# Kernel tuning notes

Measured on AMD Instinct MI355X. Metric: run time of the kernel, lower is better.

## Reference

```python
import jax, jax.numpy as jnp
import numpy as np
from jax import lax

STATE_LEN = 5
N_BASE = 4
N_STATES = N_BASE ** STATE_LEN      # 1024
ALPHA_LEN = N_BASE + 1              # 5 (blank + 4 bases)
BLANK_SCORE = 2.0
SCALE = 5.0
NEG = -1e30                         # log-zero surrogate (avoids -inf NaNs)

def _make_idx():
    s = np.arange(N_STATES)
    stay = s[:, None]
    # torch: arange(1024).repeat_interleave(4).reshape(4,-1).T -> idx[j,1+b] = b*256 + j//4
    move = np.repeat(s, N_BASE).reshape(N_BASE, -1).T
    return jnp.asarray(np.concatenate([stay, move], axis=1), dtype=jnp.int32)  # (1024,5)

IDX = _make_idx()

def _logZ_full(scores):
    # full-lattice logZ; scores (T,N,5120)
    T, N, C = scores.shape
    Ms = scores.reshape(T, N, N_STATES, ALPHA_LEN)
    def step(alpha, Mt):
        a = alpha[:, IDX]                          # (N,1024,5) gather of predecessors
        return jax.nn.logsumexp(a + Mt, axis=-1), None
    alpha0 = jnp.zeros((N, N_STATES), scores.dtype)
    alphaT, _ = lax.scan(step, alpha0, Ms)
    return jax.nn.logsumexp(alphaT, axis=-1)       # (N,)

def _prepare_ctc_scores(scores, targets):
    # scores (T,N,C), targets (N,Lmax) base ids in 1..4
    t = jnp.clip(targets - 1, 0)
    T, N, C = scores.shape
    Lmax = t.shape[1]
    n = Lmax - (STATE_LEN - 1)
    stay_idx = sum(t[:, i:n + i] * (N_BASE ** (STATE_LEN - i - 1)) for i in range(STATE_LEN)) * ALPHA_LEN
    move_idx = stay_idx[:, 1:] + t[:, :n - 1] + 1
    stay = jnp.take_along_axis(scores, jnp.broadcast_to(stay_idx[None], (T, N, n)), axis=2)
    move = jnp.take_along_axis(scores, jnp.broadcast_to(move_idx[None], (T, N, n - 1)), axis=2)
    return stay, move

def _ctc_logZ(stay, move, lens):
    # stay (T,N,L), move (T,N,L-1), lens (N,) effective kmer-path lengths
    T, N, L = stay.shape
    alpha0 = jnp.full((N, L), NEG, stay.dtype).at[:, 0].set(0.0)
    def step(alpha, sm):
        s, m = sm
        moved = jnp.pad(alpha[:, :-1] + m, ((0, 0), (1, 0)), constant_values=NEG)
        return jnp.logaddexp(alpha + s, moved), None
    alphaT, _ = lax.scan(step, alpha0, (stay, move))
    return alphaT[jnp.arange(N), lens - 1]

def setup_inputs() -> dict:
    key = jax.random.key(0)
    k1, k2, k3, k4, k5, k6 = jax.random.split(key, 6)
    B, T, D, Lmax = 16, 512, 512, 256
    hs_pad = jax.random.normal(k1, (B, T, D), dtype=jnp.float32)
    hlens = jnp.full((B,), T, dtype=jnp.int32)
    ys_pad = jax.random.randint(k2, (B, Lmax), 1, 5, dtype=jnp.int32)
    ys_lens = jax.random.randint(k3, (B,), 64, Lmax + 1, dtype=jnp.int32)
    W = jax.random.normal(k4, (4096, D), dtype=jnp.float32) * 0.02
    b = jax.random.normal(k5, (4096,), dtype=jnp.float32) * 0.01
    return {"hs_pad": hs_pad, "hlens": hlens, "ys_pad": ys_pad, "ys_lens": ys_lens, "W": W, "b": b}

def reference(hs_pad, hlens, ys_pad, ys_lens, W, b):
    x = jnp.transpose(hs_pad, (1, 0, 2))                 # (T,B,D)
    scores = jnp.tanh(x @ W.T + b) * SCALE               # (T,N,4096)
    T, N, C = scores.shape
    scores = jnp.pad(scores.reshape(T, N, C // N_BASE, N_BASE),
                     ((0, 0), (0, 0), (0, 0), (1, 0)), constant_values=BLANK_SCORE)
    scores = scores.reshape(T, N, -1).astype(jnp.float32)  # (T,N,5120)
    # normalise: subtract full-lattice logZ / T
    logZ = _logZ_full(scores)
    norm = scores - logZ[:, None] / T                    # (N,1) broadcasts over (T,N,C)
    stay, move = _prepare_ctc_scores(norm, ys_pad)
    logz = _ctc_logZ(stay, move, ys_lens + 1 - STATE_LEN)
    loss = -(logz / ys_lens.astype(scores.dtype))        # (N,) (reduction=None in forward)
    scores_bt = jnp.transpose(scores, (1, 0, 2))
    return loss, scores_bt, scores_bt
```

## Files before the change

kernel.cpp:

```cpp
#include <hip/hip_runtime.h>
#include <hip/hip_bf16.h>
#include <hip/hip_fp16.h>
#include <math.h>

#define T_STEPS 512
#define NB      16
#define D_IN    512
#define CG      4096
#define CO      5120
#define LMAX    252
#define NEGF    (-1e30f)
#define SCORES_SZ 41943040LL
#define L2E 1.4426950408889634f
#define LN2 0.6931471805599453f
#define STAYT 0.36787944117144233f

typedef __attribute__((ext_vector_type(8))) short bf16x8;
typedef __attribute__((ext_vector_type(4))) float f32x4;

__device__ __forceinline__ float tanh5(float x) {
    x = fminf(fmaxf(x, -15.f), 15.f);
    float e = __expf(2.f * x);
    return 5.f * (e - 1.f) / (e + 1.f);
}
__device__ __forceinline__ unsigned short f2bf(float v) {
    __hip_bfloat16 h = __float2bfloat16(v);
    return *reinterpret_cast<unsigned short*>(&h);
}
__device__ __forceinline__ float h2f(unsigned short s) {
    union { unsigned short u; _Float16 h; } c; c.u = s;
    return (float)c.h;
}
__device__ __forceinline__ unsigned short f2h(float v) {
    union { unsigned short u; _Float16 h; } c; c.h = (_Float16)v;
    return c.u;
}
__device__ __forceinline__ void cvt8(uint4 u, float* g) {
    g[0] = h2f((unsigned short)(u.x & 0xffff)); g[1] = h2f((unsigned short)(u.x >> 16));
    g[2] = h2f((unsigned short)(u.y & 0xffff)); g[3] = h2f((unsigned short)(u.y >> 16));
    g[4] = h2f((unsigned short)(u.z & 0xffff)); g[5] = h2f((unsigned short)(u.z >> 16));
    g[6] = h2f((unsigned short)(u.w & 0xffff)); g[7] = h2f((unsigned short)(u.w >> 16));
}
__device__ __forceinline__ void xbar() {
    __builtin_amdgcn_sched_barrier(0);
    asm volatile("s_waitcnt lgkmcnt(0)");
    __builtin_amdgcn_s_barrier();
    __builtin_amdgcn_sched_barrier(0);
}
__device__ __forceinline__ void gll16(const unsigned short* g, unsigned short* l) {
    __builtin_amdgcn_global_load_lds((const __attribute__((address_space(1))) void*)g,
                                     (__attribute__((address_space(3))) void*)l, 16, 0, 0);
}

__global__ __launch_bounds__(256) void cvt_bf16_kernel(const float* __restrict__ src,
                                                       unsigned short* __restrict__ dst,
                                                       int n4) {
    int i = blockIdx.x * 256 + threadIdx.x;
    if (i < n4) {
        float4 v = *(reinterpret_cast<const float4*>(src) + i);
        ushort4 o;
        o.x = f2bf(v.x); o.y = f2bf(v.y); o.z = f2bf(v.z); o.w = f2bf(v.w);
        *(reinterpret_cast<ushort4*>(dst) + i) = o;
    }
}

template <bool WSE>
__global__ __launch_bounds__(256) void crf_gemm_bf16(
    const unsigned short* __restrict__ A16,
    const unsigned short* __restrict__ W16,
    const float* __restrict__ bias,
    float* __restrict__ out,
    unsigned short* __restrict__ e16)
{
    __shared__ unsigned short As[128 * 64];
    __shared__ unsigned short Bs[128 * 64];
    const int tid  = threadIdx.x;
    const int lane = tid & 63;
    const int wv   = __builtin_amdgcn_readfirstlane(tid >> 6);
    const int wr   = wv >> 1, wc = wv & 1;
    const int m0   = blockIdx.y * 128;
    const int n0   = blockIdx.x * 128;
    const int wbase = tid & 192;

    f32x4 acc[4][4];
    #pragma unroll
    for (int i = 0; i < 4; ++i)
        #pragma unroll
        for (int j = 0; j < 4; ++j) acc[i][j] = (f32x4){0.f, 0.f, 0.f, 0.f};

    const int l15 = lane & 15, lj = lane >> 4, l7 = lane & 7;

    for (int k0 = 0; k0 < D_IN; k0 += 64) {
        __syncthreads();
        #pragma unroll
        for (int i = 0; i < 4; ++i) {
            const int c   = i * 256 + tid;
            const int row = c >> 3;
            const int jg  = (c & 7) ^ (row & 7);
            const unsigned short* ga = A16 + (size_t)(m0 + row) * D_IN + k0 + jg * 8;
            const unsigned short* gb = W16 + (size_t)(n0 + row) * D_IN + k0 + jg * 8;
            gll16(ga, As + (size_t)(i * 256 + wbase) * 8);
            gll16(gb, Bs + (size_t)(i * 256 + wbase) * 8);
        }
        __syncthreads();
        #pragma unroll
        for (int ks = 0; ks < 2; ++ks) {
            bf16x8 af[4], bb[4];
            #pragma unroll
            for (int mi = 0; mi < 4; ++mi) {
                const int row = wr * 64 + mi * 16 + l15;
                const int jsw = (ks * 4 + lj) ^ l7;
                af[mi] = *reinterpret_cast<const bf16x8*>(&As[row * 64 + jsw * 8]);
            }
            #pragma unroll
            for (int ni = 0; ni < 4; ++ni) {
                const int row = wc * 64 + ni * 16 + l15;
                const int jsw = (ks * 4 + lj) ^ l7;
                bb[ni] = *reinterpret_cast<const bf16x8*>(&Bs[row * 64 + jsw * 8]);
            }
            #pragma unroll
            for (int mi = 0; mi < 4; ++mi)
                #pragma unroll
                for (int ni = 0; ni < 4; ++ni)
                    acc[mi][ni] = __builtin_amdgcn_mfma_f32_16x16x32_bf16(
                        af[mi], bb[ni], acc[mi][ni], 0, 0, 0);
        }
    }

    float bv[4];
    #pragma unroll
    for (int ni = 0; ni < 4; ++ni) bv[ni] = bias[n0 + wc * 64 + ni * 16 + l15];

    #pragma unroll
    for (int mi = 0; mi < 4; ++mi) {
        #pragma unroll
        for (int r = 0; r < 4; ++r) {
            const int m = m0 + wr * 64 + mi * 16 + lj * 4 + r;
            float* r1 = out + 16 + (size_t)m * CO;
            #pragma unroll
            for (int ni = 0; ni < 4; ++ni) {
                const int n = n0 + wc * 64 + ni * 16 + l15;
                const float v = tanh5(acc[mi][ni][r] + bv[ni]);
                const int ch = (n >> 2) * 5 + (n & 3) + 1;
                r1[ch] = v;
                r1[ch + SCORES_SZ] = v;
                if ((l15 & 3) == 0) {
                    r1[ch - 1] = 2.0f;
                    r1[ch - 1 + SCORES_SZ] = 2.0f;
                }
                if (WSE) e16[(size_t)m * CG + n] = f2h(__expf(v - 3.0f));
            }
        }
    }
}

__global__ __launch_bounds__(256) void fb2_kernel(
    const unsigned short* __restrict__ e16,
    const int* __restrict__ ys_pad,
    const int* __restrict__ ys_lens,
    float* __restrict__ FA, float* __restrict__ FAe,
    float* __restrict__ FB, float* __restrict__ FBe,
    float* __restrict__ CAL, float* __restrict__ CBE)
{
    __shared__ float buf[2][1024];
    __shared__ float wmax4[4];
    __shared__ int tcl[256];
    const int role = blockIdx.x >> 4;
    const int n = blockIdx.x & 15;
    const int q = threadIdx.x;
    const int w = q >> 6, lane = q & 63;
    if (role < 2) {
        const bool FWD = (role == 0);
        const unsigned short* eb = e16 + (size_t)(n * T_STEPS) * CG + 16 * q;
        float P0 = 1.f, P1 = 1.f, P2 = 1.f, P3 = 1.f, acc = 0.f;
        *(float4*)&buf[0][4 * q] = make_float4(1.f, 1.f, 1.f, 1.f);
        uint4 pf[8][2];
        #pragma unroll
        for (int u = 0; u < 8; ++u) {
            const int row = FWD ? u : (511 - u);
            pf[u][0] = *(const uint4*)(eb + (size_t)row * CG);
            pf[u][1] = *(const uint4*)(eb + (size_t)row * CG + 8);
        }
        xbar();
        int cur = 0;
        for (int t = 0; t < 256; t += 8) {
            #pragma unroll
            for (int u = 0; u < 8; ++u) {
                float g[16];
                cvt8(pf[u][0], g);
                cvt8(pf[u][1], g + 8);
                int tn = t + u + 8; if (tn > 255) tn = 255;
                const int row = FWD ? tn : (511 - tn);
                pf[u][0] = *(const uint4*)(eb + (size_t)row * CG);
                pf[u][1] = *(const uint4*)(eb + (size_t)row * CG + 8);
                float n0, n1, n2, n3;
                if (FWD) {
                    const float b0 = buf[cur][q];
                    const float b1 = buf[cur][q + 256];
                    const float b2 = buf[cur][q + 512];
                    const float b3 = buf[cur][q + 768];
                    n0 = fmaf(STAYT, P0, fmaf(g[0],  b0, g[1]  * b1) + fmaf(g[2],  b2, g[3]  * b3));
                    n1 = fmaf(STAYT, P1, fmaf(g[4],  b0, g[5]  * b1) + fmaf(g[6],  b2, g[7]  * b3));
                    n2 = fmaf(STAYT, P2, fmaf(g[8],  b0, g[9]  * b1) + fmaf(g[10], b2, g[11] * b3));
                    n3 = fmaf(STAYT, P3, fmaf(g[12], b0, g[13] * b1) + fmaf(g[14], b2, g[15] * b3));
                } else {
                    const float4 b4 = *(const float4*)&buf[cur][4 * q];
                    n0 = fmaf(STAYT, P0, fmaf(g[0], b4.x, g[4] * b4.y) + fmaf(g[8],  b4.z, g[12] * b4.w));
                    n1 = fmaf(STAYT, P1, fmaf(g[1], b4.x, g[5] * b4.y) + fmaf(g[9],  b4.z, g[13] * b4.w));
                    n2 = fmaf(STAYT, P2, fmaf(g[2], b4.x, g[6] * b4.y) + fmaf(g[10], b4.z, g[14] * b4.w));
                    n3 = fmaf(STAYT, P3, fmaf(g[3], b4.x, g[7] * b4.y) + fmaf(g[11], b4.z, g[15] * b4.w));
                }
                if (((t + u) & 7) == 1) {
                    const float wm = fmaxf(fmaxf(wmax4[0], wmax4[1]), fmaxf(wmax4[2], wmax4[3]));
                    const int e = (int)((__float_as_uint(wm) >> 23) & 0xff) - 127;
                    const float c = __uint_as_float((unsigned)(127 - e) << 23);
                    n0 *= c; n1 *= c; n2 *= c; n3 *= c;
                    acc += (float)e;
                }
                P0 = n0; P1 = n1; P2 = n2; P3 = n3;
                if (FWD) {
                    *(float4*)&buf[cur ^ 1][4 * q] = make_float4(P0, P1, P2, P3);
                } else {
                    buf[cur ^ 1][q]       = P0;
                    buf[cur ^ 1][q + 256] = P1;
                    buf[cur ^ 1][q + 512] = P2;
                    buf[cur ^ 1][q + 768] = P3;
                }
                if (((t + u) & 7) == 0) {
                    float m = fmaxf(fmaxf(P0, P1), fmaxf(P2, P3));
                    #pragma unroll
                    for (int msk = 1; msk < 64; msk <<= 1)
                        m = fmaxf(m, __shfl_xor(m, msk, 64));
                    if (lane == 0) wmax4[w] = m;
                }
                xbar();
                cur ^= 1;
            }
        }
        if (FWD) {
            *(float4*)&FA[n * 1024 + 4 * q] = make_float4(P0, P1, P2, P3);
            if (q == 0) FAe[n] = acc;
        } else {
            FB[n * 1024 + q]       = P0;
            FB[n * 1024 + q + 256] = P1;
            FB[n * 1024 + q + 512] = P2;
            FB[n * 1024 + q + 768] = P3;
            if (q == 0) FBe[n] = acc;
        }
    } else {
        float* abuf = &buf[0][0];
        const bool FWD = (role == 2);
        tcl[q] = max(ys_pad[n * 256 + q] - 1, 0);
        xbar();
        int mch = 0; bool val;
        if (FWD) {
            val = (q >= 1 && q < LMAX);
            if (val) {
                const int code = tcl[q] * 256 + tcl[q + 1] * 64 + tcl[q + 2] * 16
                               + tcl[q + 3] * 4 + tcl[q + 4];
                mch = code * 4 + tcl[q - 1];
            }
        } else {
            val = (q < LMAX - 1);
            if (val) {
                const int code = tcl[q + 1] * 256 + tcl[q + 2] * 64 + tcl[q + 3] * 16
                               + tcl[q + 4] * 4 + tcl[q + 5];
                mch = code * 4 + tcl[q];
            }
        }
        const int li = ys_lens[n] - 5;
        float a = FWD ? ((q == 0) ? 0.f : NEGF)
                      : ((q == li) ? 0.f : NEGF);
        abuf[q] = a;
        const unsigned short* eb = e16 + (size_t)(n * T_STEPS) * CG + mch;
        unsigned short pv[16];
        #pragma unroll
        for (int s = 0; s < 16; ++s) {
            const int row = FWD ? s : (511 - s);
            pv[s] = eb[(size_t)row * CG];
        }
        xbar();
        const float STAY2 = (2.0f - 3.0f) * L2E;
        int cur = 0;
        for (int t = 0; t < 256; t += 16) {
            #pragma unroll
            for (int u = 0; u < 16; ++u) {
                const float g2 = val ? __builtin_amdgcn_logf(h2f(pv[u])) : NEGF;
                int tn = t + u + 16; if (tn > 255) tn = 255;
                const int row = FWD ? tn : (511 - tn);
                pv[u] = eb[(size_t)row * CG];
                float nb;
                if (FWD) nb = (q > 0)   ? abuf[cur * 256 + q - 1] : NEGF;
                else     nb = (q < 255) ? abuf[cur * 256 + q + 1] : NEGF;
                const float st = a + STAY2;
                const float mv = nb + g2;
                const float mx = fmaxf(st, mv);
                const float mn = fminf(st, mv);
                a = mx + __builtin_amdgcn_logf(1.f + __builtin_amdgcn_exp2f(mn - mx));
                abuf[(cur ^ 1) * 256 + q] = a;
                xbar();
                cur ^= 1;
            }
        }
        if (FWD) CAL[n * 256 + q] = a;
        else     CBE[n * 256 + q] = a;
    }
}

__global__ __launch_bounds__(256) void combine2_kernel(
    const float* __restrict__ FA, const float* __restrict__ FAe,
    const float* __restrict__ FB, const float* __restrict__ FBe,
    const float* __restrict__ CAL, const float* __restrict__ CBE,
    const int* __restrict__ ys_lens,
    float* __restrict__ out)
{
    __shared__ float red[256];
    __shared__ float lz;
    const int n = blockIdx.x;
    const int q = threadIdx.x;
    float s = 0.f;
    #pragma unroll
    for (int k = 0; k < 4; ++k)
        s += FA[n * 1024 + 4 * q + k] * FB[n * 1024 + 4 * q + k];
    red[q] = s; __syncthreads();
    for (int off = 128; off > 0; off >>= 1) {
        if (q < off) red[q] += red[q + off];
        __syncthreads();
    }
    if (q == 0) lz = FAe[n] + FBe[n] + __builtin_amdgcn_logf(red[0]);
    __syncthreads();
    const float x = CAL[n * 256 + q] + CBE[n * 256 + q];
    red[q] = x; __syncthreads();
    for (int off = 128; off > 0; off >>= 1) {
        if (q < off) red[q] = fmaxf(red[q], red[q + off]);
        __syncthreads();
    }
    const float m = red[0]; __syncthreads();
    red[q] = __builtin_amdgcn_exp2f(x - m); __syncthreads();
    for (int off = 128; off > 0; off >>= 1) {
        if (q < off) red[q] += red[q + off];
        __syncthreads();
    }
    if (q == 0) {
        const float un = m + __builtin_amdgcn_logf(red[0]);
        out[n] = -(LN2 * (un - lz) / (float)ys_lens[n]);
    }
}

__global__ __launch_bounds__(1024) void crf_fwd_kernel(
    const float* __restrict__ scores,
    const int* __restrict__ ys_pad,
    const int* __restrict__ ys_lens,
    float* __restrict__ ws)
{
    const int blk = blockIdx.x;
    const float STAY = 2.0f * L2E;
    if (blk < NB) {
        const int n = blk;
        const int s = threadIdx.x;
        __shared__ float buf[2][1024];
        __shared__ float red[1024];
        float alpha = 0.f;
        buf[0][s] = 0.f;
        const int j0 = s >> 2;
        const float* rowp = scores + (size_t)(n * T_STEPS) * CO + 5 * s + 1;
        float pm[4][4];
        #pragma unroll
        for (int u = 0; u < 4; ++u) {
            const float* r = rowp + (size_t)u * CO;
            pm[u][0] = r[0]; pm[u][1] = r[1]; pm[u][2] = r[2]; pm[u][3] = r[3];
        }
        __syncthreads();
        int cur = 0;
        for (int t = 0; t < T_STEPS; t += 4) {
            #pragma unroll
            for (int u = 0; u < 4; ++u) {
                const float m1 = pm[u][0], m2 = pm[u][1], m3 = pm[u][2], m4 = pm[u][3];
                int tp = t + u + 4; if (tp > T_STEPS - 1) tp = T_STEPS - 1;
                const float* r = rowp + (size_t)tp * CO;
                pm[u][0] = r[0]; pm[u][1] = r[1]; pm[u][2] = r[2]; pm[u][3] = r[3];
                const float b1 = buf[cur][j0];
                const float b2 = buf[cur][j0 + 256];
                const float b3 = buf[cur][j0 + 512];
                const float b4 = buf[cur][j0 + 768];
                const float a0 = alpha + STAY;
                const float a1 = fmaf(m1, L2E, b1);
                const float a2 = fmaf(m2, L2E, b2);
                const float a3 = fmaf(m3, L2E, b3);
                const float a4 = fmaf(m4, L2E, b4);
                const float mx = fmaxf(fmaxf(fmaxf(a0, a1), fmaxf(a2, a3)), a4);
                const float sum = __builtin_amdgcn_exp2f(a0 - mx) + __builtin_amdgcn_exp2f(a1 - mx)
                                + __builtin_amdgcn_exp2f(a2 - mx) + __builtin_amdgcn_exp2f(a3 - mx)
                                + __builtin_amdgcn_exp2f(a4 - mx);
                alpha = mx + __builtin_amdgcn_logf(sum);
                buf[cur ^ 1][s] = alpha;
                __syncthreads();
                cur ^= 1;
            }
        }
        red[s] = alpha;
        __syncthreads();
        for (int off = 512; off > 0; off >>= 1) {
            if (s < off) red[s] = fmaxf(red[s], red[s + off]);
            __syncthreads();
        }
        const float gmax = red[0];
        __syncthreads();
        red[s] = __builtin_amdgcn_exp2f(alpha - gmax);
        __syncthreads();
        for (int off = 512; off > 0; off >>= 1) {
            if (s < off) red[s] += red[s + off];
            __syncthreads();
        }
        if (s == 0) ws[n] = LN2 * (gmax + __builtin_amdgcn_logf(red[0]));
    } else {
        const int n = blk - NB;
        const int i = threadIdx.x;
        __shared__ float abuf[2][LMAX];
        __shared__ int tcl[256];
        if (i < 256) tcl[i] = max(ys_pad[n * 256 + i] - 1, 0);
        __syncthreads();
        int mch = -1;
        if (i >= 1 && i < LMAX) {
            const int code = tcl[i] * 256 + tcl[i + 1] * 64 + tcl[i + 2] * 16
                           + tcl[i + 3] * 4 + tcl[i + 4];
            mch = code * 5 + tcl[i - 1] + 1;
        }
        float alpha = (i == 0) ? 0.f : NEGF;
        if (i < LMAX) abuf[0][i] = alpha;
        const float* base = scores + (size_t)(n * T_STEPS) * CO;
        const size_t moff = (mch >= 0) ? (size_t)mch : 0;
        float pg[4];
        #pragma unroll
        for (int u = 0; u < 4; ++u) pg[u] = base[(size_t)u * CO + moff];
        __syncthreads();
        int cur = 0;
        for (int t = 0; t < T_STEPS; t += 4) {
            #pragma unroll
            for (int u = 0; u < 4; ++u) {
                const float g = pg[u];
                int tp = t + u + 4; if (tp > T_STEPS - 1) tp = T_STEPS - 1;
                pg[u] = base[(size_t)tp * CO + moff];
                if (i < LMAX) {
                    const float a_stay = alpha + STAY;
                    const float prev = (i > 0) ? abuf[cur][i - 1] : NEGF;
                    const float a_mv = (i > 0) ? fmaf(g, L2E, prev) : NEGF;
                    const float mx = fmaxf(a_stay, a_mv);
                    const float mn = fminf(a_stay, a_mv);
                    alpha = mx + __builtin_amdgcn_logf(1.f + __builtin_amdgcn_exp2f(mn - mx));
                    abuf[cur ^ 1][i] = alpha;
                }
                __syncthreads();
                cur ^= 1;
            }
        }
        if (i == ys_lens[n] - 5) ws[NB + n] = alpha * LN2;
    }
}

__global__ void crf_loss_kernel(const float* __restrict__ ws,
                                const int* __restrict__ ys_lens,
                                float* __restrict__ out)
{
    const int n = threadIdx.x;
    if (n < NB) {
        const float logz = ws[NB + n] - ws[n];
        out[n] = -(logz / (float)ys_lens[n]);
    }
}

extern "C" void kernel_launch(void* const* d_in, const int* in_sizes, int n_in,
                              void* d_out, int out_size, void* d_ws, size_t ws_size,
                              hipStream_t stream)
{
    const float* hs      = (const float*)d_in[0];
    const int*   ys_pad  = (const int*)d_in[2];
    const int*   ys_lens = (const int*)d_in[3];
    const float* W       = (const float*)d_in[4];
    const float* bias    = (const float*)d_in[5];
    float* out = (float*)d_out;
    float* ws  = (float*)d_ws;

    const size_t A_ELEMS = (size_t)8192 * 512;
    const size_t W_ELEMS = (size_t)4096 * 512;
    const size_t E_ELEMS = (size_t)8192 * 4096;
    const size_t X_FLOATS = (size_t)16 * 1024 * 2 + 32 + (size_t)16 * 256 * 2;
    const size_t NEED = 256 + (A_ELEMS + W_ELEMS + E_ELEMS) * 2 + X_FLOATS * 4;

    unsigned short* A16 = (unsigned short*)((char*)d_ws + 256);
    unsigned short* W16 = A16 + A_ELEMS;
    unsigned short* E16 = W16 + W_ELEMS;
    float* FA  = (float*)(E16 + E_ELEMS);
    float* FAe = FA + 16 * 1024;
    float* FB  = FAe + 16;
    float* FBe = FB + 16 * 1024;
    float* CAL = FBe + 16;
    float* CBE = CAL + 16 * 256;

    cvt_bf16_kernel<<<(int)(A_ELEMS / 4 / 256), 256, 0, stream>>>(hs, A16, (int)(A_ELEMS / 4));
    cvt_bf16_kernel<<<(int)(W_ELEMS / 4 / 256), 256, 0, stream>>>(W, W16, (int)(W_ELEMS / 4));
    dim3 grid(CG / 128, (NB * T_STEPS) / 128);

    if (ws_size >= NEED) {
        crf_gemm_bf16<true><<<grid, 256, 0, stream>>>(A16, W16, bias, out, E16);
        fb2_kernel<<<64, 256, 0, stream>>>(E16, ys_pad, ys_lens, FA, FAe, FB, FBe, CAL, CBE);
        combine2_kernel<<<16, 256, 0, stream>>>(FA, FAe, FB, FBe, CAL, CBE, ys_lens, out);
    } else {
        crf_gemm_bf16<false><<<grid, 256, 0, stream>>>(A16, W16, bias, out, nullptr);
        crf_fwd_kernel<<<2 * NB, 1024, 0, stream>>>(out + 16, ys_pad, ys_lens, ws);
        crf_loss_kernel<<<1, 64, 0, stream>>>(ws, ys_lens, out);
    }
}
```

Before: 214.0 us.

## Write time-reversed exp-score copy so backward passes stream forward; shrink prefetch depth

The GEMM epilogue now writes a second fp16 exp-score buffer with time reversed within each sequence, so the backward recurrences read rows in ascending address order, like the forward ones. The prefetch depth in the recurrence kernels drops (8 to 4 rows, 16 to 4 values), and the custom barrier is replaced with __syncthreads. This aims to simplify addressing and lower register pressure in the latency-bound scans. It doubles the GEMM's fp16 side writes (an extra 64MB) and the workspace size.

Result: slower. 243.8 us (+14.0%).

```diff
diff --git a/kernel.cpp b/kernel.cpp
--- a/kernel.cpp
+++ b/kernel.cpp
@@ -41,12 +41,6 @@
     g[4] = h2f((unsigned short)(u.z & 0xffff)); g[5] = h2f((unsigned short)(u.z >> 16));
     g[6] = h2f((unsigned short)(u.w & 0xffff)); g[7] = h2f((unsigned short)(u.w >> 16));
 }
-__device__ __forceinline__ void xbar() {
-    __builtin_amdgcn_sched_barrier(0);
-    asm volatile("s_waitcnt lgkmcnt(0)");
-    __builtin_amdgcn_s_barrier();
-    __builtin_amdgcn_sched_barrier(0);
-}
 __device__ __forceinline__ void gll16(const unsigned short* g, unsigned short* l) {
     __builtin_amdgcn_global_load_lds((const __attribute__((address_space(1))) void*)g,
                                      (__attribute__((address_space(3))) void*)l, 16, 0, 0);
@@ -70,7 +64,8 @@
     const unsigned short* __restrict__ W16,
     const float* __restrict__ bias,
     float* __restrict__ out,
-    unsigned short* __restrict__ e16)
+    unsigned short* __restrict__ e16,
+    unsigned short* __restrict__ e16r)
 {
     __shared__ unsigned short As[128 * 64];
     __shared__ unsigned short Bs[128 * 64];
@@ -136,6 +131,8 @@
         #pragma unroll
         for (int r = 0; r < 4; ++r) {
             const int m = m0 + wr * 64 + mi * 16 + lj * 4 + r;
+            const int bt = m & 511;
+            const size_t mrev = (size_t)(m - bt) + (511 - bt);
             float* r1 = out + 16 + (size_t)m * CO;
             #pragma unroll
             for (int ni = 0; ni < 4; ++ni) {
@@ -148,14 +145,19 @@
                     r1[ch - 1] = 2.0f;
                     r1[ch - 1 + SCORES_SZ] = 2.0f;
                 }
-                if (WSE) e16[(size_t)m * CG + n] = f2h(__expf(v - 3.0f));
-            }
-        }
-    }
-}
-
-__global__ __launch_bounds__(256) void fb2_kernel(
+                if (WSE) {
+                    const unsigned short ev = f2h(__expf(v - 3.0f));
+                    e16[(size_t)m * CG + n] = ev;
+                    e16r[mrev * CG + n] = ev;
+                }
+            }
+        }
+    }
+}
+
+__global__ __launch_bounds__(256) void fb4_kernel(
     const unsigned short* __restrict__ e16,
+    const unsigned short* __restrict__ e16r,
     const int* __restrict__ ys_pad,
     const int* __restrict__ ys_lens,
     float* __restrict__ FA, float* __restrict__ FAe,
@@ -171,28 +173,26 @@
     const int w = q >> 6, lane = q & 63;
     if (role < 2) {
         const bool FWD = (role == 0);
-        const unsigned short* eb = e16 + (size_t)(n * T_STEPS) * CG + 16 * q;
+        const unsigned short* eb = (FWD ? e16 : e16r) + (size_t)(n * T_STEPS) * CG + 16 * q;
         float P0 = 1.f, P1 = 1.f, P2 = 1.f, P3 = 1.f, acc = 0.f;
         *(float4*)&buf[0][4 * q] = make_float4(1.f, 1.f, 1.f, 1.f);
-        uint4 pf[8][2];
-        #pragma unroll
-        for (int u = 0; u < 8; ++u) {
-            const int row = FWD ? u : (511 - u);
-            pf[u][0] = *(const uint4*)(eb + (size_t)row * CG);
-            pf[u][1] = *(const uint4*)(eb + (size_t)row * CG + 8);
-        }
-        xbar();
+        uint4 pf[4][2];
+        #pragma unroll
+        for (int u = 0; u < 4; ++u) {
+            pf[u][0] = *(const uint4*)(eb + (size_t)u * CG);
+            pf[u][1] = *(const uint4*)(eb + (size_t)u * CG + 8);
+        }
+        __syncthreads();
         int cur = 0;
         for (int t = 0; t < 256; t += 8) {
             #pragma unroll
             for (int u = 0; u < 8; ++u) {
                 float g[16];
-                cvt8(pf[u][0], g);
-                cvt8(pf[u][1], g + 8);
-                int tn = t + u + 8; if (tn > 255) tn = 255;
-                const int row = FWD ? tn : (511 - tn);
-                pf[u][0] = *(const uint4*)(eb + (size_t)row * CG);
-                pf[u][1] = *(const uint4*)(eb + (size_t)row * CG + 8);
+                cvt8(pf[u & 3][0], g);
+                cvt8(pf[u & 3][1], g + 8);
+                int tp = t + u + 4; if (tp > 255) tp = 255;
+                pf[u & 3][0] = *(const uint4*)(eb + (size_t)tp * CG);
+                pf[u & 3][1] = *(const uint4*)(eb + (size_t)tp * CG + 8);
                 float n0, n1, n2, n3;
                 if (FWD) {
                     const float b0 = buf[cur][q];
@@ -210,7 +210,7 @@
                     n2 = fmaf(STAYT, P2, fmaf(g[2], b4.x, g[6] * b4.y) + fmaf(g[10], b4.z, g[14] * b4.w));
                     n3 = fmaf(STAYT, P3, fmaf(g[3], b4.x, g[7] * b4.y) + fmaf(g[11], b4.z, g[15] * b4.w));
                 }
-                if (((t + u) & 7) == 1) {
+                if (u == 1) {
                     const float wm = fmaxf(fmaxf(wmax4[0], wmax4[1]), fmaxf(wmax4[2], wmax4[3]));
                     const int e = (int)((__float_as_uint(wm) >> 23) & 0xff) - 127;
                     const float c = __uint_as_float((unsigned)(127 - e) << 23);
@@ -226,14 +226,14 @@
                     buf[cur ^ 1][q + 512] = P2;
                     buf[cur ^ 1][q + 768] = P3;
                 }
-                if (((t + u) & 7) == 0) {
+                if (u == 0) {
                     float m = fmaxf(fmaxf(P0, P1), fmaxf(P2, P3));
                     #pragma unroll
                     for (int msk = 1; msk < 64; msk <<= 1)
                         m = fmaxf(m, __shfl_xor(m, msk, 64));
                     if (lane == 0) wmax4[w] = m;
                 }
-                xbar();
+                __syncthreads();
                 cur ^= 1;
             }
         }
@@ -248,10 +248,9 @@
             if (q == 0) FBe[n] = acc;
         }
     } else {
-        float* abuf = &buf[0][0];
         const bool FWD = (role == 2);
         tcl[q] = max(ys_pad[n * 256 + q] - 1, 0);
-        xbar();
+        __syncthreads();
         int mch = 0; bool val;
         if (FWD) {
             val = (q >= 1 && q < LMAX);
@@ -271,34 +270,30 @@
         const int li = ys_lens[n] - 5;
         float a = FWD ? ((q == 0) ? 0.f : NEGF)
                       : ((q == li) ? 0.f : NEGF);
-        abuf[q] = a;
-        const unsigned short* eb = e16 + (size_t)(n * T_STEPS) * CG + mch;
-        unsigned short pv[16];
-        #pragma unroll
-        for (int s = 0; s < 16; ++s) {
-            const int row = FWD ? s : (511 - s);
-            pv[s] = eb[(size_t)row * CG];
-        }
-        xbar();
+        buf[0][q] = a;
+        const unsigned short* eb = (FWD ? e16 : e16r) + (size_t)(n * T_STEPS) * CG + mch;
+        unsigned short pv[4];
+        #pragma unroll
+        for (int u = 0; u < 4; ++u) pv[u] = eb[(size_t)u * CG];
+        __syncthreads();
         const float STAY2 = (2.0f - 3.0f) * L2E;
         int cur = 0;
-        for (int t = 0; t < 256; t += 16) {
-            #pragma unroll
-            for (int u = 0; u < 16; ++u) {
+        for (int t = 0; t < 256; t += 4) {
+            #pragma unroll
+            for (int u = 0; u < 4; ++u) {
                 const float g2 = val ? __builtin_amdgcn_logf(h2f(pv[u])) : NEGF;
-                int tn = t + u + 16; if (tn > 255) tn = 255;
-                const int row = FWD ? tn : (511 - tn);
-                pv[u] = eb[(size_t)row * CG];
+                int tp = t + u + 4; if (tp > 255) tp = 255;
+                pv[u] = eb[(size_t)tp * CG];
                 float nb;
-                if (FWD) nb = (q > 0)   ? abuf[cur * 256 + q - 1] : NEGF;
-                else     nb = (q < 255) ? abuf[cur * 256 + q + 1] : NEGF;
+                if (FWD) nb = (q > 0)   ? buf[cur][q - 1] : NEGF;
+                else     nb = (q < 255) ? buf[cur][q + 1] : NEGF;
                 const float st = a + STAY2;
                 const float mv = nb + g2;
                 const float mx = fmaxf(st, mv);
                 const float mn = fminf(st, mv);
                 a = mx + __builtin_amdgcn_logf(1.f + __builtin_amdgcn_exp2f(mn - mx));
-                abuf[(cur ^ 1) * 256 + q] = a;
-                xbar();
+                buf[cur ^ 1][q] = a;
+                __syncthreads();
                 cur ^= 1;
             }
         }
@@ -485,12 +480,13 @@
     const size_t W_ELEMS = (size_t)4096 * 512;
     const size_t E_ELEMS = (size_t)8192 * 4096;
     const size_t X_FLOATS = (size_t)16 * 1024 * 2 + 32 + (size_t)16 * 256 * 2;
-    const size_t NEED = 256 + (A_ELEMS + W_ELEMS + E_ELEMS) * 2 + X_FLOATS * 4;
-
-    unsigned short* A16 = (unsigned short*)((char*)d_ws + 256);
-    unsigned short* W16 = A16 + A_ELEMS;
-    unsigned short* E16 = W16 + W_ELEMS;
-    float* FA  = (float*)(E16 + E_ELEMS);
+    const size_t NEED = 256 + (A_ELEMS + W_ELEMS + 2 * E_ELEMS) * 2 + X_FLOATS * 4;
+
+    unsigned short* A16  = (unsigned short*)((char*)d_ws + 256);
+    unsigned short* W16  = A16 + A_ELEMS;
+    unsigned short* E16  = W16 + W_ELEMS;
+    unsigned short* E16R = E16 + E_ELEMS;
+    float* FA  = (float*)(E16R + E_ELEMS);
     float* FAe = FA + 16 * 1024;
     float* FB  = FAe + 16;
     float* FBe = FB + 16 * 1024;
@@ -502,11 +498,11 @@
     dim3 grid(CG / 128, (NB * T_STEPS) / 128);
 
     if (ws_size >= NEED) {
-        crf_gemm_bf16<true><<<grid, 256, 0, stream>>>(A16, W16, bias, out, E16);
-        fb2_kernel<<<64, 256, 0, stream>>>(E16, ys_pad, ys_lens, FA, FAe, FB, FBe, CAL, CBE);
+        crf_gemm_bf16<true><<<grid, 256, 0, stream>>>(A16, W16, bias, out, E16, E16R);
+        fb4_kernel<<<64, 256, 0, stream>>>(E16, E16R, ys_pad, ys_lens, FA, FAe, FB, FBe, CAL, CBE);
         combine2_kernel<<<16, 256, 0, stream>>>(FA, FAe, FB, FBe, CAL, CBE, ys_lens, out);
     } else {
-        crf_gemm_bf16<false><<<grid, 256, 0, stream>>>(A16, W16, bias, out, nullptr);
+        crf_gemm_bf16<false><<<grid, 256, 0, stream>>>(A16, W16, bias, out, nullptr, nullptr);
         crf_fwd_kernel<<<2 * NB, 1024, 0, stream>>>(out + 16, ys_pad, ys_lens, ws);
         crf_loss_kernel<<<1, 64, 0, stream>>>(ws, ys_lens, out);
     }
```

## Fuse GEMM and forward-backward recurrences into one kernel with tile completion flags

Applied to the files above, without the earlier changes.

The GEMM and the sequential forward/backward recurrence kernel are merged into one persistent launch. The first 64 blocks run the recurrences and spin on per-tile atomic counters, and the remaining 2048 blocks compute GEMM tiles, ordered so the time-blocks the scans need first are produced first. The goal is to overlap the latency-bound scans with GEMM work instead of serialising the two. This relies on the recurrence blocks being co-resident with the GEMM blocks and on release/acquire fences being correct. Spinning blocks also occupy CUs and add a memset launch.

New measurement: 435.7 us. 104% more time.

```diff
diff --git a/kernel.cpp b/kernel.cpp
--- a/kernel.cpp
+++ b/kernel.cpp
@@ -51,6 +51,14 @@
     __builtin_amdgcn_global_load_lds((const __attribute__((address_space(1))) void*)g,
                                      (__attribute__((address_space(3))) void*)l, 16, 0, 0);
 }
+__device__ __forceinline__ void wait_tile(unsigned int* done, int idx) {
+    if (threadIdx.x == 0) {
+        while (__hip_atomic_load(&done[idx], __ATOMIC_RELAXED, __HIP_MEMORY_SCOPE_AGENT) < 32u)
+            __builtin_amdgcn_s_sleep(8);
+    }
+    __syncthreads();
+    __builtin_amdgcn_fence(__ATOMIC_ACQUIRE, "agent");
+}
 
 __global__ __launch_bounds__(256) void cvt_bf16_kernel(const float* __restrict__ src,
                                                        unsigned short* __restrict__ dst,
@@ -64,116 +72,131 @@
     }
 }
 
-template <bool WSE>
-__global__ __launch_bounds__(256) void crf_gemm_bf16(
+__global__ __launch_bounds__(256) void mega_kernel(
     const unsigned short* __restrict__ A16,
     const unsigned short* __restrict__ W16,
     const float* __restrict__ bias,
     float* __restrict__ out,
-    unsigned short* __restrict__ e16)
-{
-    __shared__ unsigned short As[128 * 64];
-    __shared__ unsigned short Bs[128 * 64];
-    const int tid  = threadIdx.x;
-    const int lane = tid & 63;
-    const int wv   = __builtin_amdgcn_readfirstlane(tid >> 6);
-    const int wr   = wv >> 1, wc = wv & 1;
-    const int m0   = blockIdx.y * 128;
-    const int n0   = blockIdx.x * 128;
-    const int wbase = tid & 192;
-
-    f32x4 acc[4][4];
-    #pragma unroll
-    for (int i = 0; i < 4; ++i)
-        #pragma unroll
-        for (int j = 0; j < 4; ++j) acc[i][j] = (f32x4){0.f, 0.f, 0.f, 0.f};
-
-    const int l15 = lane & 15, lj = lane >> 4, l7 = lane & 7;
-
-    for (int k0 = 0; k0 < D_IN; k0 += 64) {
-        __syncthreads();
-        #pragma unroll
-        for (int i = 0; i < 4; ++i) {
-            const int c   = i * 256 + tid;
-            const int row = c >> 3;
-            const int jg  = (c & 7) ^ (row & 7);
-            const unsigned short* ga = A16 + (size_t)(m0 + row) * D_IN + k0 + jg * 8;
-            const unsigned short* gb = W16 + (size_t)(n0 + row) * D_IN + k0 + jg * 8;
-            gll16(ga, As + (size_t)(i * 256 + wbase) * 8);
-            gll16(gb, Bs + (size_t)(i * 256 + wbase) * 8);
-        }
-        __syncthreads();
-        #pragma unroll
-        for (int ks = 0; ks < 2; ++ks) {
-            bf16x8 af[4], bb[4];
-            #pragma unroll
-            for (int mi = 0; mi < 4; ++mi) {
-                const int row = wr * 64 + mi * 16 + l15;
-                const int jsw = (ks * 4 + lj) ^ l7;
-                af[mi] = *reinterpret_cast<const bf16x8*>(&As[row * 64 + jsw * 8]);
-            }
-            #pragma unroll
-            for (int ni = 0; ni < 4; ++ni) {
-                const int row = wc * 64 + ni * 16 + l15;
-                const int jsw = (ks * 4 + lj) ^ l7;
-                bb[ni] = *reinterpret_cast<const bf16x8*>(&Bs[row * 64 + jsw * 8]);
-            }
-            #pragma unroll
-            for (int mi = 0; mi < 4; ++mi)
-                #pragma unroll
-                for (int ni = 0; ni < 4; ++ni)
-                    acc[mi][ni] = __builtin_amdgcn_mfma_f32_16x16x32_bf16(
-                        af[mi], bb[ni], acc[mi][ni], 0, 0, 0);
-        }
-    }
-
-    float bv[4];
-    #pragma unroll
-    for (int ni = 0; ni < 4; ++ni) bv[ni] = bias[n0 + wc * 64 + ni * 16 + l15];
-
-    #pragma unroll
-    for (int mi = 0; mi < 4; ++mi) {
-        #pragma unroll
-        for (int r = 0; r < 4; ++r) {
-            const int m = m0 + wr * 64 + mi * 16 + lj * 4 + r;
-            float* r1 = out + 16 + (size_t)m * CO;
-            #pragma unroll
-            for (int ni = 0; ni < 4; ++ni) {
-                const int n = n0 + wc * 64 + ni * 16 + l15;
-                const float v = tanh5(acc[mi][ni][r] + bv[ni]);
-                const int ch = (n >> 2) * 5 + (n & 3) + 1;
-                r1[ch] = v;
-                r1[ch + SCORES_SZ] = v;
-                if ((l15 & 3) == 0) {
-                    r1[ch - 1] = 2.0f;
-                    r1[ch - 1 + SCORES_SZ] = 2.0f;
-                }
-                if (WSE) e16[(size_t)m * CG + n] = f2h(__expf(v - 3.0f));
-            }
-        }
-    }
-}
-
-__global__ __launch_bounds__(256) void fb2_kernel(
-    const unsigned short* __restrict__ e16,
+    unsigned short* __restrict__ e16,
     const int* __restrict__ ys_pad,
     const int* __restrict__ ys_lens,
+    unsigned int* __restrict__ done,
     float* __restrict__ FA, float* __restrict__ FAe,
     float* __restrict__ FB, float* __restrict__ FBe,
     float* __restrict__ CAL, float* __restrict__ CBE)
 {
-    __shared__ float buf[2][1024];
-    __shared__ float wmax4[4];
-    __shared__ int tcl[256];
+    __shared__ unsigned char SH[32896];
+    const int tid = threadIdx.x;
+
+    if (blockIdx.x >= 64) {
+        unsigned short* As = (unsigned short*)SH;
+        unsigned short* Bs = (unsigned short*)(SH + 16384);
+        const int g = blockIdx.x - 64;
+        const int prio = g >> 9;
+        const int nb   = (g >> 5) & 15;
+        const int x    = g & 31;
+        const int tb   = (int)((0u | (3u << 2) | (1u << 4) | (2u << 6)) >> (2 * prio)) & 3;
+        const int m0   = nb * 512 + tb * 128;
+        const int n0   = x * 128;
+        const int lane = tid & 63;
+        const int wv   = __builtin_amdgcn_readfirstlane(tid >> 6);
+        const int wr   = wv >> 1, wc = wv & 1;
+        const int wbase = tid & 192;
+
+        f32x4 acc[4][4];
+        #pragma unroll
+        for (int i = 0; i < 4; ++i)
+            #pragma unroll
+            for (int j = 0; j < 4; ++j) acc[i][j] = (f32x4){0.f, 0.f, 0.f, 0.f};
+
+        const int l15 = lane & 15, lj = lane >> 4, l7 = lane & 7;
+
+        for (int k0 = 0; k0 < D_IN; k0 += 64) {
+            __syncthreads();
+            #pragma unroll
+            for (int i = 0; i < 4; ++i) {
+                const int c   = i * 256 + tid;
+                const int row = c >> 3;
+                const int jg  = (c & 7) ^ (row & 7);
+                const unsigned short* ga = A16 + (size_t)(m0 + row) * D_IN + k0 + jg * 8;
+                const unsigned short* gb = W16 + (size_t)(n0 + row) * D_IN + k0 + jg * 8;
+                gll16(ga, As + (size_t)(i * 256 + wbase) * 8);
+                gll16(gb, Bs + (size_t)(i * 256 + wbase) * 8);
+            }
+            __syncthreads();
+            #pragma unroll
+            for (int ks = 0; ks < 2; ++ks) {
+                bf16x8 af[4], bb[4];
+                #pragma unroll
+                for (int mi = 0; mi < 4; ++mi) {
+                    const int row = wr * 64 + mi * 16 + l15;
+                    const int jsw = (ks * 4 + lj) ^ l7;
+                    af[mi] = *reinterpret_cast<const bf16x8*>(&As[row * 64 + jsw * 8]);
+                }
+                #pragma unroll
+                for (int ni = 0; ni < 4; ++ni) {
+                    const int row = wc * 64 + ni * 16 + l15;
+                    const int jsw = (ks * 4 + lj) ^ l7;
+                    bb[ni] = *reinterpret_cast<const bf16x8*>(&Bs[row * 64 + jsw * 8]);
+                }
+                #pragma unroll
+                for (int mi = 0; mi < 4; ++mi)
+                    #pragma unroll
+                    for (int ni = 0; ni < 4; ++ni)
+                        acc[mi][ni] = __builtin_amdgcn_mfma_f32_16x16x32_bf16(
+                            af[mi], bb[ni], acc[mi][ni], 0, 0, 0);
+            }
+        }
+
+        float bv[4];
+        #pragma unroll
+        for (int ni = 0; ni < 4; ++ni) bv[ni] = bias[n0 + wc * 64 + ni * 16 + l15];
+
+        #pragma unroll
+        for (int mi = 0; mi < 4; ++mi) {
+            #pragma unroll
+            for (int r = 0; r < 4; ++r) {
+                const int m = m0 + wr * 64 + mi * 16 + lj * 4 + r;
+                float* r1 = out + 16 + (size_t)m * CO;
+                #pragma unroll
+                for (int ni = 0; ni < 4; ++ni) {
+                    const int n = n0 + wc * 64 + ni * 16 + l15;
+                    const float v = tanh5(acc[mi][ni][r] + bv[ni]);
+                    const int ch = (n >> 2) * 5 + (n & 3) + 1;
+                    r1[ch] = v;
+                    r1[ch + SCORES_SZ] = v;
+                    if ((l15 & 3) == 0) {
+                        r1[ch - 1] = 2.0f;
+                        r1[ch - 1 + SCORES_SZ] = 2.0f;
+                    }
+                    e16[(size_t)m * CG + n] = f2h(__expf(v - 3.0f));
+                }
+            }
+        }
+        __syncthreads();
+        if (tid == 0) {
+            __builtin_amdgcn_fence(__ATOMIC_RELEASE, "agent");
+            __hip_atomic_fetch_add(&done[nb * 4 + tb], 1u,
+                                   __ATOMIC_RELAXED, __HIP_MEMORY_SCOPE_AGENT);
+        }
+        return;
+    }
+
+    float (*buf)[1024] = (float(*)[1024])SH;
+    float* wmax4 = (float*)(SH + 8192);
+    int*   tcl   = (int*)(SH + 8208);
     const int role = blockIdx.x >> 4;
     const int n = blockIdx.x & 15;
-    const int q = threadIdx.x;
+    const int q = tid;
     const int w = q >> 6, lane = q & 63;
+    const bool FWD = !(role & 1);
+
     if (role < 2) {
-        const bool FWD = (role == 0);
         const unsigned short* eb = e16 + (size_t)(n * T_STEPS) * CG + 16 * q;
         float P0 = 1.f, P1 = 1.f, P2 = 1.f, P3 = 1.f, acc = 0.f;
         *(float4*)&buf[0][4 * q] = make_float4(1.f, 1.f, 1.f, 1.f);
+        int have = FWD ? 0 : 3;
+        wait_tile(done, n * 4 + have);
         uint4 pf[8][2];
         #pragma unroll
         for (int u = 0; u < 8; ++u) {
@@ -184,6 +207,11 @@
         xbar();
         int cur = 0;
         for (int t = 0; t < 256; t += 8) {
+            {
+                const int la = (t + 11 < 255) ? (t + 11) : 255;
+                const int tbo = FWD ? (la >> 7) : ((511 - la) >> 7);
+                if (tbo != have) { wait_tile(done, n * 4 + tbo); have = tbo; }
+            }
             #pragma unroll
             for (int u = 0; u < 8; ++u) {
                 float g[16];
@@ -249,7 +277,6 @@
         }
     } else {
         float* abuf = &buf[0][0];
-        const bool FWD = (role == 2);
         tcl[q] = max(ys_pad[n * 256 + q] - 1, 0);
         xbar();
         int mch = 0; bool val;
@@ -272,6 +299,8 @@
         float a = FWD ? ((q == 0) ? 0.f : NEGF)
                       : ((q == li) ? 0.f : NEGF);
         abuf[q] = a;
+        int have = FWD ? 0 : 3;
+        wait_tile(done, n * 4 + have);
         const unsigned short* eb = e16 + (size_t)(n * T_STEPS) * CG + mch;
         unsigned short pv[16];
         #pragma unroll
@@ -283,6 +312,11 @@
         const float STAY2 = (2.0f - 3.0f) * L2E;
         int cur = 0;
         for (int t = 0; t < 256; t += 16) {
+            {
+                const int la = (t + 31 < 255) ? (t + 31) : 255;
+                const int tbo = FWD ? (la >> 7) : ((511 - la) >> 7);
+                if (tbo != have) { wait_tile(done, n * 4 + tbo); have = tbo; }
+            }
             #pragma unroll
             for (int u = 0; u < 16; ++u) {
                 const float g2 = val ? __builtin_amdgcn_logf(h2f(pv[u])) : NEGF;
@@ -344,6 +378,88 @@
     if (q == 0) {
         const float un = m + __builtin_amdgcn_logf(red[0]);
         out[n] = -(LN2 * (un - lz) / (float)ys_lens[n]);
+    }
+}
+
+__global__ __launch_bounds__(256) void crf_gemm_fallback(
+    const unsigned short* __restrict__ A16,
+    const unsigned short* __restrict__ W16,
+    const float* __restrict__ bias,
+    float* __restrict__ out)
+{
+    __shared__ unsigned short As[128 * 64];
+    __shared__ unsigned short Bs[128 * 64];
+    const int tid  = threadIdx.x;
+    const int lane = tid & 63;
+    const int wv   = __builtin_amdgcn_readfirstlane(tid >> 6);
+    const int wr   = wv >> 1, wc = wv & 1;
+    const int m0   = blockIdx.y * 128;
+    const int n0   = blockIdx.x * 128;
+    const int wbase = tid & 192;
+    f32x4 acc[4][4];
+    #pragma unroll
+    for (int i = 0; i < 4; ++i)
+        #pragma unroll
+        for (int j = 0; j < 4; ++j) acc[i][j] = (f32x4){0.f, 0.f, 0.f, 0.f};
+    const int l15 = lane & 15, lj = lane >> 4, l7 = lane & 7;
+    for (int k0 = 0; k0 < D_IN; k0 += 64) {
+        __syncthreads();
+        #pragma unroll
+        for (int i = 0; i < 4; ++i) {
+            const int c   = i * 256 + tid;
+            const int row = c >> 3;
+            const int jg  = (c & 7) ^ (row & 7);
+            const unsigned short* ga = A16 + (size_t)(m0 + row) * D_IN + k0 + jg * 8;
+            const unsigned short* gb = W16 + (size_t)(n0 + row) * D_IN + k0 + jg * 8;
+            gll16(ga, As + (size_t)(i * 256 + wbase) * 8);
+            gll16(gb, Bs + (size_t)(i * 256 + wbase) * 8);
+        }
+        __syncthreads();
+        #pragma unroll
+        for (int ks = 0; ks < 2; ++ks) {
+            bf16x8 af[4], bb[4];
+            #pragma unroll
+            for (int mi = 0; mi < 4; ++mi) {
+                const int row = wr * 64 + mi * 16 + l15;
+                const int jsw = (ks * 4 + lj) ^ l7;
+                af[mi] = *reinterpret_cast<const bf16x8*>(&As[row * 64 + jsw * 8]);
+            }
+            #pragma unroll
+            for (int ni = 0; ni < 4; ++ni) {
+                const int row = wc * 64 + ni * 16 + l15;
+                const int jsw = (ks * 4 + lj) ^ l7;
+                bb[ni] = *reinterpret_cast<const bf16x8*>(&Bs[row * 64 + jsw * 8]);
+            }
+            #pragma unroll
+            for (int mi = 0; mi < 4; ++mi)
+                #pragma unroll
+                for (int ni = 0; ni < 4; ++ni)
+                    acc[mi][ni] = __builtin_amdgcn_mfma_f32_16x16x32_bf16(
+                        af[mi], bb[ni], acc[mi][ni], 0, 0, 0);
+        }
+    }
+    float bv[4];
+    #pragma unroll
+    for (int ni = 0; ni < 4; ++ni) bv[ni] = bias[n0 + wc * 64 + ni * 16 + l15];
+    #pragma unroll
+    for (int mi = 0; mi < 4; ++mi) {
+        #pragma unroll
+        for (int r = 0; r < 4; ++r) {
+            const int m = m0 + wr * 64 + mi * 16 + lj * 4 + r;
+            float* r1 = out + 16 + (size_t)m * CO;
+            #pragma unroll
+            for (int ni = 0; ni < 4; ++ni) {
+                const int n = n0 + wc * 64 + ni * 16 + l15;
+                const float v = tanh5(acc[mi][ni][r] + bv[ni]);
+                const int ch = (n >> 2) * 5 + (n & 3) + 1;
+                r1[ch] = v;
+                r1[ch + SCORES_SZ] = v;
+                if ((l15 & 3) == 0) {
+                    r1[ch - 1] = 2.0f;
+                    r1[ch - 1 + SCORES_SZ] = 2.0f;
+                }
+            }
+        }
     }
 }
 
@@ -487,6 +603,7 @@
     const size_t X_FLOATS = (size_t)16 * 1024 * 2 + 32 + (size_t)16 * 256 * 2;
     const size_t NEED = 256 + (A_ELEMS + W_ELEMS + E_ELEMS) * 2 + X_FLOATS * 4;
 
+    unsigned int* done = (unsigned int*)d_ws;
     unsigned short* A16 = (unsigned short*)((char*)d_ws + 256);
     unsigned short* W16 = A16 + A_ELEMS;
     unsigned short* E16 = W16 + W_ELEMS;
@@ -499,14 +616,16 @@
 
     cvt_bf16_kernel<<<(int)(A_ELEMS / 4 / 256), 256, 0, stream>>>(hs, A16, (int)(A_ELEMS / 4));
     cvt_bf16_kernel<<<(int)(W_ELEMS / 4 / 256), 256, 0, stream>>>(W, W16, (int)(W_ELEMS / 4));
-    dim3 grid(CG / 128, (NB * T_STEPS) / 128);
 
     if (ws_size >= NEED) {
-        crf_gemm_bf16<true><<<grid, 256, 0, stream>>>(A16, W16, bias, out, E16);
-        fb2_kernel<<<64, 256, 0, stream>>>(E16, ys_pad, ys_lens, FA, FAe, FB, FBe, CAL, CBE);
+        hipMemsetAsync(d_ws, 0, 256, stream);
+        mega_kernel<<<64 + 2048, 256, 0, stream>>>(A16, W16, bias, out, E16,
+                                                   ys_pad, ys_lens, done,
+                                                   FA, FAe, FB, FBe, CAL, CBE);
         combine2_kernel<<<16, 256, 0, stream>>>(FA, FAe, FB, FBe, CAL, CBE, ys_lens, out);
     } else {
-        crf_gemm_bf16<false><<<grid, 256, 0, stream>>>(A16, W16, bias, out, nullptr);
+        dim3 grid(CG / 128, (NB * T_STEPS) / 128);
+        crf_gemm_fallback<<<grid, 256, 0, stream>>>(A16, W16, bias, out);
         crf_fwd_kernel<<<2 * NB, 1024, 0, stream>>>(out + 16, ys_pad, ys_lens, ws);
         crf_loss_kernel<<<1, 64, 0, stream>>>(ws, ys_lens, out);
     }
```
